# Optimization experiments

Measured on AMD Instinct MI355X. Metric: run time of the kernel, lower is better.

## Reference

```python
import jax, jax.numpy as jnp
import numpy as np

HEADS = 16  # must match init kwarg


def setup_inputs() -> dict:
    key = jax.random.key(0)
    k0, k1, k2, k3 = jax.random.split(key, 4)
    D = 1024       # dim
    N_SENTS = 32
    N_ENTS = 32
    SE = N_SENTS * N_ENTS  # sents_x_ents = 1024
    B = 64
    entities = jax.random.normal(k0, (SE, B, D), dtype=jnp.float32)
    padding_mask = jnp.zeros((SE, B), dtype=jnp.bool_)  # True = do not attend
    # learned parameters (torch.nn.MultiheadAttention layout)
    query = jax.random.uniform(k1, (D,), jnp.float32, -1.0, 1.0)  # nn.init.uniform_(-1, 1)
    in_proj_w = jax.random.normal(k2, (3 * D, D), jnp.float32) / np.float32(np.sqrt(D))
    in_proj_b = jnp.zeros((3 * D,), jnp.float32)
    out_proj_w = jax.random.normal(k3, (D, D), jnp.float32) / np.float32(np.sqrt(D))
    out_proj_b = jnp.zeros((D,), jnp.float32)
    return {
        'entities': entities,
        'padding_mask': padding_mask,
        'n_sents': N_SENTS,
        'query': query,
        'in_proj_w': in_proj_w,
        'in_proj_b': in_proj_b,
        'out_proj_w': out_proj_w,
        'out_proj_b': out_proj_b,
    }


def reference(entities, padding_mask, n_sents, query, in_proj_w, in_proj_b,
              out_proj_w, out_proj_b):
    SE, B, D = entities.shape
    n_ents = SE // n_sents
    H = HEADS
    hd = D // H
    scale = 1.0 / np.float32(np.sqrt(hd))

    Wq, Wk, Wv = in_proj_w[:D], in_proj_w[D:2 * D], in_proj_w[2 * D:]
    bq, bk, bv = in_proj_b[:D], in_proj_b[D:2 * D], in_proj_b[2 * D:]

    # Single shared query vector (the torch module expands query to all
    # n_sents x batch positions, so q is identical everywhere).
    q = ((query @ Wq.T + bq) * scale).reshape(H, hd)          # [H, hd]

    # K / V projections: the dominant GEMMs.
    k = (entities @ Wk.T + bk).reshape(n_sents, n_ents, B, H, hd)
    v = (entities @ Wv.T + bv).reshape(n_sents, n_ents, B, H, hd)

    # Block-diagonal attention: query s attends only to its own n_ents block.
    scores = jnp.einsum('hd,sebhd->sbhe', q, k)               # [S, B, H, E]

    pm = jnp.transpose(padding_mask.reshape(n_sents, n_ents, B), (0, 2, 1))  # [S, B, E]
    scores = jnp.where(pm[:, :, None, :], -jnp.inf, scores)
    attn = jax.nn.softmax(scores, axis=-1)                    # [S, B, H, E]

    ctx = jnp.einsum('sbhe,sebhd->sbhd', attn, v).reshape(n_sents, B, D)
    result = ctx @ out_proj_w.T + out_proj_b                  # [S, B, D]

    # Fully-masked blocks produce NaN in torch; the module zero-fills them.
    all_masked = jnp.all(pm, axis=2)                          # [S, B]
    result = jnp.where(all_masked[:, :, None], 0.0, result)
    return result
```

## Files before the change

### kernel.cpp

```cpp
#include <hip/hip_runtime.h>
#include <hip/hip_bf16.h>

#define NS 32
#define NE 32
#define BB 64
#define DD 1024
#define HH 16
#define SB (NS * BB)

typedef __attribute__((ext_vector_type(4))) float f32x4;
typedef __attribute__((ext_vector_type(8))) short short8;

static __device__ __forceinline__ unsigned short f2bf(float f) {
  union { float f; unsigned int u; } c{f};
  unsigned int u = c.u;
  return (unsigned short)((u + 0x7FFFu + ((u >> 16) & 1u)) >> 16);
}

static __device__ __forceinline__ unsigned int pk2bf(float a, float b) {
  __hip_bfloat162 h = __float22bfloat162_rn(float2{a, b});
  union { __hip_bfloat162 h; unsigned int u; } c{h};
  return c.u;
}

extern "C" __global__ __launch_bounds__(256)
void k0_prep(const float* __restrict__ ipw, const float* __restrict__ ipb,
             const float* __restrict__ query, const float* __restrict__ opw,
             unsigned short* __restrict__ rT, unsigned short* __restrict__ wv,
             unsigned short* __restrict__ wo) {
  __shared__ float qh[64];
  const int blk = blockIdx.x;
  const int t = threadIdx.x;
  if (blk < 64) {
    const int h = blk >> 2, dpart = blk & 3;
    const int wu = t >> 6, ln = t & 63;
    for (int jj = 0; jj < 16; ++jj) {
      int j = wu * 16 + jj;
      const float* row = ipw + (size_t)(h * 64 + j) * DD;
      float s = 0.f;
      for (int k = ln; k < DD; k += 64) s += row[k] * query[k];
      #pragma unroll
      for (int off = 32; off; off >>= 1) s += __shfl_xor(s, off);
      if (ln == 0) qh[j] = (s + ipb[h * 64 + j]) * 0.125f;
    }
    __syncthreads();
    const float* wk = ipw + (size_t)DD * DD;
    const int d = dpart * 256 + t;
    float s = 0.f;
    #pragma unroll 8
    for (int j = 0; j < 64; ++j)
      s += qh[j] * wk[(size_t)(h * 64 + j) * DD + d];
    rT[h * DD + d] = f2bf(s);
  } else {
    const int i = (blk - 64) * 256 + t;
    const float* wv_f = ipw + (size_t)2 * DD * DD;
    if (i < 262144) {
      float4 v = reinterpret_cast<const float4*>(wv_f)[i];
      reinterpret_cast<uint2*>(wv)[i] = uint2{pk2bf(v.x, v.y), pk2bf(v.z, v.w)};
    } else {
      const int j = i - 262144;
      float4 v = reinterpret_cast<const float4*>(opw)[j];
      reinterpret_cast<uint2*>(wo)[j] = uint2{pk2bf(v.x, v.y), pk2bf(v.z, v.w)};
    }
  }
}

extern "C" __global__ __launch_bounds__(512, 4)
void k1_scores_agg(const float* __restrict__ ent,
                   const unsigned char* __restrict__ mask,
                   const unsigned short* __restrict__ rT,
                   unsigned short* __restrict__ agg,
                   unsigned char* __restrict__ flags) {
  __shared__ unsigned short elds[NE * DD];
  __shared__ float slds[NE][HH];
  __shared__ unsigned short attnT[HH][NE];
  __shared__ unsigned char mlds[NE];

  const int sb = blockIdx.x;
  const int s = sb >> 6, b = sb & 63;
  const int t = threadIdx.x;
  const int lane = t & 63;
  const int wave = t >> 6;

  const float* base = ent + ((size_t)(s * NE) * BB + b) * DD;
  #pragma unroll
  for (int i = 0; i < 16; ++i) {
    int f4 = t + 512 * i;
    int e = f4 >> 8;
    int d0 = (f4 & 255) << 2;
    float4 v = *reinterpret_cast<const float4*>(base + (size_t)e * (BB * DD) + d0);
    int sidx = ((e << 10) + d0) ^ ((e & 7) << 3);
    *reinterpret_cast<uint2*>(&elds[sidx]) = uint2{pk2bf(v.x, v.y), pk2bf(v.z, v.w)};
  }
  if (t < NE) mlds[t] = mask[(size_t)(s * NE + t) * BB + b];
  __syncthreads();

  if (wave < 2) {
    const int g = lane >> 4, m = lane & 15;
    const int e = wave * 16 + m;
    f32x4 acc = {0.f, 0.f, 0.f, 0.f};
    #pragma unroll 4
    for (int ks = 0; ks < 32; ++ks) {
      int d0 = (ks << 5) + (g << 3);
      short8 a = *reinterpret_cast<const short8*>(&elds[((e << 10) + d0) ^ ((e & 7) << 3)]);
      short8 bb = *reinterpret_cast<const short8*>(rT + (m << 10) + d0);
      acc = __builtin_amdgcn_mfma_f32_16x16x32_bf16(a, bb, acc, 0, 0, 0);
    }
    #pragma unroll
    for (int r = 0; r < 4; ++r)
      slds[wave * 16 + (g << 2) + r][m] = acc[r];
  }
  __syncthreads();

  {
    const int h = t >> 5, e = t & 31;
    bool msk = mlds[e] != 0;
    float v = msk ? -3.4e38f : slds[e][h];
    float mx = v;
    #pragma unroll
    for (int off = 16; off; off >>= 1) mx = fmaxf(mx, __shfl_xor(mx, off));
    float ex = msk ? 0.f : __expf(v - mx);
    float sm = ex;
    #pragma unroll
    for (int off = 16; off; off >>= 1) sm += __shfl_xor(sm, off);
    float at = sm > 0.f ? ex / sm : 0.f;
    attnT[h][e] = f2bf(at);
  }
  if (t == 0) {
    unsigned char all = 1;
    for (int e = 0; e < NE; ++e) all &= (mlds[e] ? (unsigned char)1 : (unsigned char)0);
    flags[sb] = all;
  }
  __syncthreads();

  {
    const int g = lane >> 4, c = lane & 15;
    short8 a = *reinterpret_cast<const short8*>(&attnT[c][g << 3]);
    unsigned short* ob = agg + ((size_t)sb << 14);
    #pragma unroll
    for (int q = 0; q < 8; ++q) {
      const int nt = (wave << 3) + q;
      const int d = (nt << 4) + c;
      short8 bb;
      #pragma unroll
      for (int j = 0; j < 8; ++j) {
        int e = (g << 3) + j;
        bb[j] = (short)elds[((e << 10) + d) ^ ((e & 7) << 3)];
      }
      f32x4 acc = {0.f, 0.f, 0.f, 0.f};
      acc = __builtin_amdgcn_mfma_f32_16x16x32_bf16(a, bb, acc, 0, 0, 0);
      #pragma unroll
      for (int r = 0; r < 4; ++r)
        ob[(((g << 2) + r) << 10) + d] = f2bf(acc[r]);
    }
  }
}

extern "C" __global__ __launch_bounds__(256, 4)
void k2_ctx(const unsigned short* __restrict__ agg,
            const unsigned short* __restrict__ wv,
            const float* __restrict__ bv,
            unsigned short* __restrict__ ctx) {
  const int mt = blockIdx.x;
  const int h = blockIdx.y;
  const int t = threadIdx.x, lane = t & 63, wave = t >> 6;
  const int g = lane >> 4, c = lane & 15;
  const int row0 = mt * 64 + wave * 16;
  f32x4 acc[4] = {{0,0,0,0},{0,0,0,0},{0,0,0,0},{0,0,0,0}};
  #pragma unroll 2
  for (int ks = 0; ks < 32; ++ks) {
    int k0 = (ks << 5) + (g << 3);
    short8 a = *reinterpret_cast<const short8*>(agg + ((size_t)((row0 + c) * 16 + h) << 10) + k0);
    #pragma unroll
    for (int nt = 0; nt < 4; ++nt) {
      short8 bb = *reinterpret_cast<const short8*>(wv + ((size_t)(h * 64 + nt * 16 + c) << 10) + k0);
      acc[nt] = __builtin_amdgcn_mfma_f32_16x16x32_bf16(a, bb, acc[nt], 0, 0, 0);
    }
  }
  #pragma unroll
  for (int nt = 0; nt < 4; ++nt)
    #pragma unroll
    for (int r = 0; r < 4; ++r) {
      int col = h * 64 + nt * 16 + c;
      ctx[((size_t)(row0 + (g << 2) + r) << 10) + col] = f2bf(acc[nt][r] + bv[col]);
    }
}

extern "C" __global__ __launch_bounds__(256, 4)
void k3_out(const unsigned short* __restrict__ ctx,
            const unsigned short* __restrict__ wo,
            const float* __restrict__ bias,
            const unsigned char* __restrict__ flags,
            float* __restrict__ out) {
  const int mt = blockIdx.x;
  const int n0 = blockIdx.y * 64;
  const int t = threadIdx.x, lane = t & 63, wave = t >> 6;
  const int g = lane >> 4, c = lane & 15;
  const int row0 = mt * 64 + wave * 16;
  f32x4 acc[4] = {{0,0,0,0},{0,0,0,0},{0,0,0,0},{0,0,0,0}};
  #pragma unroll 2
  for (int ks = 0; ks < 32; ++ks) {
    int k0 = (ks << 5) + (g << 3);
    short8 a = *reinterpret_cast<const short8*>(ctx + ((size_t)(row0 + c) << 10) + k0);
    #pragma unroll
    for (int nt = 0; nt < 4; ++nt) {
      short8 bb = *reinterpret_cast<const short8*>(wo + ((size_t)(n0 + nt * 16 + c) << 10) + k0);
      acc[nt] = __builtin_amdgcn_mfma_f32_16x16x32_bf16(a, bb, acc[nt], 0, 0, 0);
    }
  }
  #pragma unroll
  for (int nt = 0; nt < 4; ++nt)
    #pragma unroll
    for (int r = 0; r < 4; ++r) {
      int row = row0 + (g << 2) + r;
      int col = n0 + nt * 16 + c;
      float v = acc[nt][r] + bias[col];
      if (flags[row]) v = 0.f;
      out[(size_t)row * DD + col] = v;
    }
}

extern "C" void kernel_launch(void* const* d_in, const int* in_sizes, int n_in,
                              void* d_out, int out_size, void* d_ws, size_t ws_size,
                              hipStream_t stream) {
  const float* ent = (const float*)d_in[0];
  const unsigned char* mask = (const unsigned char*)d_in[1];
  const float* query = (const float*)d_in[3];
  const float* ipw = (const float*)d_in[4];
  const float* ipb = (const float*)d_in[5];
  const float* opw = (const float*)d_in[6];
  const float* opb = (const float*)d_in[7];
  float* out = (float*)d_out;

  char* ws = (char*)d_ws;
  unsigned char* flags = (unsigned char*)(ws + 4096);
  unsigned short* rT = (unsigned short*)(ws + 8192);
  unsigned short* wv = (unsigned short*)(ws + 65536);
  unsigned short* wo = (unsigned short*)(ws + 65536 + (2u << 20));
  unsigned short* ctx = (unsigned short*)(ws + 65536 + (4u << 20));
  unsigned short* agg = (unsigned short*)(ws + 65536 + (8u << 20));

  hipLaunchKernelGGL(k0_prep, dim3(64 + 2048), dim3(256), 0, stream,
                     ipw, ipb, query, opw, rT, wv, wo);
  hipLaunchKernelGGL(k1_scores_agg, dim3(SB), dim3(512), 0, stream,
                     ent, mask, rT, agg, flags);
  hipLaunchKernelGGL(k2_ctx, dim3(32, 16), dim3(256), 0, stream,
                     agg, wv, ipb + 2 * DD, ctx);
  hipLaunchKernelGGL(k3_out, dim3(32, 16), dim3(256), 0, stream,
                     ctx, wo, opb, flags, out);
}
```

Baseline: 617.6 us.

## Split score MFMA across all waves, stage agg via LDS, transpose agg for k2

The score GEMM in k1 is now split across all 8 waves along K, with partial sums written to padded LDS and added together, where previously only 2 waves did the work. The aggregated output is first staged in LDS and then written with coalesced 64-bit stores in a head-major [H][SB][D] layout. k2 loads contiguous 64x256 tiles of this transposed layout into swizzled LDS, replacing strided global reads. This adds extra syncthreads and LDS traffic, and k2 now needs 32KB of LDS, which may lower occupancy.

```diff
diff --git a/kernel.cpp b/kernel.cpp
--- a/kernel.cpp
+++ b/kernel.cpp
@@ -69,10 +69,10 @@
 void k1_scores_agg(const float* __restrict__ ent,
                    const unsigned char* __restrict__ mask,
                    const unsigned short* __restrict__ rT,
-                   unsigned short* __restrict__ agg,
+                   unsigned short* __restrict__ aggT,
                    unsigned char* __restrict__ flags) {
   __shared__ unsigned short elds[NE * DD];
-  __shared__ float slds[NE][HH];
+  __shared__ float sldsp[4][NE][HH + 1];
   __shared__ unsigned short attnT[HH][NE];
   __shared__ unsigned char mlds[NE];
 
@@ -81,6 +81,7 @@
   const int t = threadIdx.x;
   const int lane = t & 63;
   const int wave = t >> 6;
+  const int g = lane >> 4;
 
   const float* base = ent + ((size_t)(s * NE) * BB + b) * DD;
   #pragma unroll
@@ -95,12 +96,14 @@
   if (t < NE) mlds[t] = mask[(size_t)(s * NE + t) * BB + b];
   __syncthreads();
 
-  if (wave < 2) {
-    const int g = lane >> 4, m = lane & 15;
-    const int e = wave * 16 + m;
+  {
+    const int m = lane & 15;
+    const int et = wave & 1, kq = wave >> 1;
+    const int e = et * 16 + m;
     f32x4 acc = {0.f, 0.f, 0.f, 0.f};
-    #pragma unroll 4
-    for (int ks = 0; ks < 32; ++ks) {
+    #pragma unroll
+    for (int i = 0; i < 8; ++i) {
+      int ks = kq * 8 + i;
       int d0 = (ks << 5) + (g << 3);
       short8 a = *reinterpret_cast<const short8*>(&elds[((e << 10) + d0) ^ ((e & 7) << 3)]);
       short8 bb = *reinterpret_cast<const short8*>(rT + (m << 10) + d0);
@@ -108,14 +111,15 @@
     }
     #pragma unroll
     for (int r = 0; r < 4; ++r)
-      slds[wave * 16 + (g << 2) + r][m] = acc[r];
+      sldsp[kq][et * 16 + (g << 2) + r][m] = acc[r];
   }
   __syncthreads();
 
   {
     const int h = t >> 5, e = t & 31;
     bool msk = mlds[e] != 0;
-    float v = msk ? -3.4e38f : slds[e][h];
+    float v = msk ? -3.4e38f
+                  : (sldsp[0][e][h] + sldsp[1][e][h] + sldsp[2][e][h] + sldsp[3][e][h]);
     float mx = v;
     #pragma unroll
     for (int off = 16; off; off >>= 1) mx = fmaxf(mx, __shfl_xor(mx, off));
@@ -133,10 +137,10 @@
   }
   __syncthreads();
 
-  {
-    const int g = lane >> 4, c = lane & 15;
+  f32x4 qacc[8];
+  {
+    const int c = lane & 15;
     short8 a = *reinterpret_cast<const short8*>(&attnT[c][g << 3]);
-    unsigned short* ob = agg + ((size_t)sb << 14);
     #pragma unroll
     for (int q = 0; q < 8; ++q) {
       const int nt = (wave << 3) + q;
@@ -147,36 +151,75 @@
         int e = (g << 3) + j;
         bb[j] = (short)elds[((e << 10) + d) ^ ((e & 7) << 3)];
       }
-      f32x4 acc = {0.f, 0.f, 0.f, 0.f};
-      acc = __builtin_amdgcn_mfma_f32_16x16x32_bf16(a, bb, acc, 0, 0, 0);
+      f32x4 z = {0.f, 0.f, 0.f, 0.f};
+      qacc[q] = __builtin_amdgcn_mfma_f32_16x16x32_bf16(a, bb, z, 0, 0, 0);
+    }
+  }
+  __syncthreads();
+
+  {
+    const int c = lane & 15;
+    #pragma unroll
+    for (int q = 0; q < 8; ++q) {
+      const int d = (((wave << 3) + q) << 4) + c;
       #pragma unroll
       for (int r = 0; r < 4; ++r)
-        ob[(((g << 2) + r) << 10) + d] = f2bf(acc[r]);
+        elds[(((g << 2) + r) << 10) + d] = f2bf(qacc[q][r]);
+    }
+  }
+  __syncthreads();
+  {
+    const unsigned long long* src64 = reinterpret_cast<const unsigned long long*>(elds);
+    #pragma unroll
+    for (int p = 0; p < 8; ++p) {
+      int off = p * 512 + t;
+      int h = off >> 8;
+      int d = (off << 2) & 1023;
+      *reinterpret_cast<unsigned long long*>(
+          aggT + (((size_t)h * SB + sb) << 10) + d) = src64[off];
     }
   }
 }
 
 extern "C" __global__ __launch_bounds__(256, 4)
-void k2_ctx(const unsigned short* __restrict__ agg,
+void k2_ctx(const unsigned short* __restrict__ aggT,
             const unsigned short* __restrict__ wv,
             const float* __restrict__ bv,
             unsigned short* __restrict__ ctx) {
+  __shared__ unsigned short alds[64 * 256];
   const int mt = blockIdx.x;
   const int h = blockIdx.y;
-  const int t = threadIdx.x, lane = t & 63, wave = t >> 6;
+  const int t = threadIdx.x, lane = t & 63, w = t >> 6;
   const int g = lane >> 4, c = lane & 15;
-  const int row0 = mt * 64 + wave * 16;
+  const char* abase = reinterpret_cast<const char*>(aggT + (((size_t)h * SB + mt * 64) << 10));
   f32x4 acc[4] = {{0,0,0,0},{0,0,0,0},{0,0,0,0},{0,0,0,0}};
-  #pragma unroll 2
-  for (int ks = 0; ks < 32; ++ks) {
-    int k0 = (ks << 5) + (g << 3);
-    short8 a = *reinterpret_cast<const short8*>(agg + ((size_t)((row0 + c) * 16 + h) << 10) + k0);
-    #pragma unroll
-    for (int nt = 0; nt < 4; ++nt) {
-      short8 bb = *reinterpret_cast<const short8*>(wv + ((size_t)(h * 64 + nt * 16 + c) << 10) + k0);
-      acc[nt] = __builtin_amdgcn_mfma_f32_16x16x32_bf16(a, bb, acc[nt], 0, 0, 0);
-    }
-  }
+  for (int kc = 0; kc < 4; ++kc) {
+    __syncthreads();
+    #pragma unroll
+    for (int it = 0; it < 8; ++it) {
+      int o = it * 4096 + t * 16;
+      int row = o >> 9;
+      int inb = o & 511;
+      uint4 v = *reinterpret_cast<const uint4*>(abase + (size_t)row * 2048 + kc * 512 + inb);
+      *reinterpret_cast<uint4*>(
+          reinterpret_cast<char*>(alds) + row * 512 + (inb ^ ((row & 7) << 4))) = v;
+    }
+    __syncthreads();
+    #pragma unroll
+    for (int ks = 0; ks < 8; ++ks) {
+      int row = w * 16 + c;
+      int inb = (ks * 32 + g * 8) * 2;
+      short8 a = *reinterpret_cast<const short8*>(
+          reinterpret_cast<const char*>(alds) + row * 512 + (inb ^ ((row & 7) << 4)));
+      int kg = kc * 256 + ks * 32 + g * 8;
+      #pragma unroll
+      for (int nt = 0; nt < 4; ++nt) {
+        short8 bb = *reinterpret_cast<const short8*>(wv + ((size_t)(h * 64 + nt * 16 + c) << 10) + kg);
+        acc[nt] = __builtin_amdgcn_mfma_f32_16x16x32_bf16(a, bb, acc[nt], 0, 0, 0);
+      }
+    }
+  }
+  const int row0 = mt * 64 + w * 16;
   #pragma unroll
   for (int nt = 0; nt < 4; ++nt)
     #pragma unroll
@@ -238,14 +281,14 @@
   unsigned short* wv = (unsigned short*)(ws + 65536);
   unsigned short* wo = (unsigned short*)(ws + 65536 + (2u << 20));
   unsigned short* ctx = (unsigned short*)(ws + 65536 + (4u << 20));
-  unsigned short* agg = (unsigned short*)(ws + 65536 + (8u << 20));
+  unsigned short* aggT = (unsigned short*)(ws + 65536 + (8u << 20));
 
   hipLaunchKernelGGL(k0_prep, dim3(64 + 2048), dim3(256), 0, stream,
                      ipw, ipb, query, opw, rT, wv, wo);
   hipLaunchKernelGGL(k1_scores_agg, dim3(SB), dim3(512), 0, stream,
-                     ent, mask, rT, agg, flags);
+                     ent, mask, rT, aggT, flags);
   hipLaunchKernelGGL(k2_ctx, dim3(32, 16), dim3(256), 0, stream,
-                     agg, wv, ipb + 2 * DD, ctx);
+                     aggT, wv, ipb + 2 * DD, ctx);
   hipLaunchKernelGGL(k3_out, dim3(32, 16), dim3(256), 0, stream,
                      ctx, wo, opb, flags, out);
 }
```

After: 593.3 us. -3.9%, faster.
